# Kernel optimization log

Hardware: AMD Instinct MI355X
Metric: run time of the kernel (lower is better)

## Reference

```python
import jax, jax.numpy as jnp
import numpy as np

C, W, H = 256, 64, 192
RECORD_LEN = np.array([5, 3, 4, 2, 5, 3, 4, 2], dtype=np.int64)  # sums to 28


def setup_inputs() -> dict:
    key = jax.random.key(0)
    total = int(RECORD_LEN.sum())
    x = jax.random.normal(key, (total, C, W, H), dtype=jnp.float32)
    record_len = jnp.asarray(RECORD_LEN)
    return {"x": x, "record_len": record_len}


def _group_attention(xx):
    # xx: [L, C, W, H] -> per-pixel self-attention over the L agents, d_model = C
    L = xx.shape[0]
    q = xx.reshape(L, C, W * H).transpose(2, 0, 1)          # [N=W*H, L, C]
    score = jnp.einsum('nlc,nmc->nlm', q, q) / jnp.sqrt(jnp.float32(C))
    attn = jax.nn.softmax(score, axis=-1)                    # [N, L, L]
    # original keeps only ego agent (row 0) of the context
    ctx0 = jnp.einsum('nm,nmc->nc', attn[:, 0, :], q)        # [N, C]
    out = ctx0.T.reshape(1, C, W, H)
    attn_maps = attn.transpose(1, 2, 0).reshape(L, L, W, H)
    return out, attn_maps


def reference(x, record_len):
    rl = np.asarray(record_len)  # static ragged lengths
    offsets = np.concatenate([[0], np.cumsum(rl)])
    outs = []
    attn_last = None
    for i in range(len(rl)):  # small fixed number of ragged groups
        xx = x[int(offsets[i]):int(offsets[i + 1])]
        out_i, attn_last = _group_attention(xx)
        outs.append(out_i)
    # matches torch: returns fused ego features per scene + attn of LAST group
    return jnp.concatenate(outs, axis=0), attn_last
```

## Files before the change

kernel.cpp:

```cpp
#include <hip/hip_runtime.h>
#include <hip/hip_bf16.h>
#include <math.h>

#define C_DIM 256
#define W_DIM 64
#define H_DIM 192
#define WH (W_DIM * H_DIM)
#define NGROUPS 8
#define BLOCKS_PER_GROUP (WH / 256)

template <int L, bool WRITE_ATTN>
__device__ __forceinline__ void att_group_body(
    const float* __restrict__ xg,
    float* __restrict__ out,
    float* __restrict__ attn_out,
    int n)
{
    constexpr int NTRI = L * (L + 1) / 2;
    float s[NTRI];
#pragma unroll
    for (int i = 0; i < NTRI; ++i) s[i] = 0.0f;

#pragma unroll 4
    for (int c = 0; c < C_DIM; ++c) {
        float v[L];
#pragma unroll
        for (int l = 0; l < L; ++l)
            v[l] = xg[(l * C_DIM + c) * WH + n];
        int idx = 0;
#pragma unroll
        for (int l = 0; l < L; ++l)
#pragma unroll
            for (int m = l; m < L; ++m)
                s[idx++] += v[l] * v[m];
    }

    const float scale = 0.0625f;

    float p0[L];
    float mx = -INFINITY;
#pragma unroll
    for (int m = 0; m < L; ++m) {
        p0[m] = s[m] * scale;
        mx = fmaxf(mx, p0[m]);
    }
    float sum = 0.0f;
#pragma unroll
    for (int m = 0; m < L; ++m) {
        p0[m] = __expf(p0[m] - mx);
        sum += p0[m];
    }
    const float inv = 1.0f / sum;
#pragma unroll
    for (int m = 0; m < L; ++m) p0[m] *= inv;

    if constexpr (WRITE_ATTN) {
        float g[L][L];
        int idx = 0;
#pragma unroll
        for (int l = 0; l < L; ++l)
#pragma unroll
            for (int m = l; m < L; ++m) {
                const float v = s[idx++] * scale;
                g[l][m] = v;
                g[m][l] = v;
            }
#pragma unroll
        for (int l = 0; l < L; ++l) {
            float mx2 = -INFINITY;
#pragma unroll
            for (int m = 0; m < L; ++m) mx2 = fmaxf(mx2, g[l][m]);
            float e[L];
            float sm = 0.0f;
#pragma unroll
            for (int m = 0; m < L; ++m) {
                e[m] = __expf(g[l][m] - mx2);
                sm += e[m];
            }
            const float iv = 1.0f / sm;
#pragma unroll
            for (int m = 0; m < L; ++m)
                attn_out[(l * L + m) * WH + n] = e[m] * iv;
        }
    }

#pragma unroll 4
    for (int c = 0; c < C_DIM; ++c) {
        float acc = 0.0f;
#pragma unroll
        for (int m = 0; m < L; ++m)
            acc += p0[m] * xg[(m * C_DIM + c) * WH + n];
        out[c * WH + n] = acc;
    }
}

__global__ __launch_bounds__(256) void att_fused_kernel(
    const float* __restrict__ x,
    float* __restrict__ out0,
    float* __restrict__ attn)
{
    const int b = blockIdx.x;
    const int g = b / BLOCKS_PER_GROUP;
    const int bn = b - g * BLOCKS_PER_GROUP;
    const int n = bn * 256 + threadIdx.x;

    const int offs[NGROUPS] = {0, 5, 8, 12, 14, 19, 22, 26};
    const int lens[NGROUPS] = {5, 3, 4, 2, 5, 3, 4, 2};

    const float* xg = x + (size_t)offs[g] * C_DIM * WH;
    float* og = out0 + (size_t)g * C_DIM * WH;

    switch (lens[g]) {
        case 5: att_group_body<5, false>(xg, og, nullptr, n); break;
        case 4: att_group_body<4, false>(xg, og, nullptr, n); break;
        case 3: att_group_body<3, false>(xg, og, nullptr, n); break;
        case 2:
            if (g == NGROUPS - 1)
                att_group_body<2, true>(xg, og, attn, n);
            else
                att_group_body<2, false>(xg, og, nullptr, n);
            break;
    }
}

extern "C" void kernel_launch(void* const* d_in, const int* in_sizes, int n_in,
                              void* d_out, int out_size, void* d_ws, size_t ws_size,
                              hipStream_t stream) {
    const float* x = (const float*)d_in[0];
    float* out0 = (float*)d_out;
    float* attn = out0 + (size_t)NGROUPS * C_DIM * WH;

    const dim3 grid(NGROUPS * BLOCKS_PER_GROUP);
    const dim3 block(256);
    att_fused_kernel<<<grid, block, 0, stream>>>(x, out0, attn);
}
```

Before: 564.9 us.

## Rewrite as persistent cooperative kernel splitting channels across blocks with flag sync

```diff
diff --git a/kernel.cpp b/kernel.cpp
--- a/kernel.cpp
+++ b/kernel.cpp
@@ -1,125 +1,296 @@
 #include <hip/hip_runtime.h>
-#include <hip/hip_bf16.h>
 #include <math.h>
 
 #define C_DIM 256
-#define W_DIM 64
-#define H_DIM 192
-#define WH (W_DIM * H_DIM)
+#define WH 12288
+#define WH4 3072
 #define NGROUPS 8
-#define BLOCKS_PER_GROUP (WH / 256)
-
-template <int L, bool WRITE_ATTN>
-__device__ __forceinline__ void att_group_body(
-    const float* __restrict__ xg,
-    float* __restrict__ out,
-    float* __restrict__ attn_out,
-    int n)
+#define STEPS 12
+#define NBLOCKS 256
+#define SLOT_V4 160
+#define SCALE 0.0625f
+
+typedef float v4 __attribute__((ext_vector_type(4)));
+
+__device__ __forceinline__ v4 v4max(v4 a, v4 b) {
+    v4 r; r[0]=fmaxf(a[0],b[0]); r[1]=fmaxf(a[1],b[1]);
+    r[2]=fmaxf(a[2],b[2]); r[3]=fmaxf(a[3],b[3]); return r;
+}
+__device__ __forceinline__ v4 v4exp(v4 a) {
+    v4 r; r[0]=__expf(a[0]); r[1]=__expf(a[1]);
+    r[2]=__expf(a[2]); r[3]=__expf(a[3]); return r;
+}
+
+__device__ __forceinline__ void load_slab(
+    v4 (&sl)[5][2], const v4* __restrict__ x4, int item, int cl, int nsub)
 {
-    constexpr int NTRI = L * (L + 1) / 2;
-    float s[NTRI];
-#pragma unroll
-    for (int i = 0; i < NTRI; ++i) s[i] = 0.0f;
-
-#pragma unroll 4
-    for (int c = 0; c < C_DIM; ++c) {
-        float v[L];
-#pragma unroll
-        for (int l = 0; l < L; ++l)
-            v[l] = xg[(l * C_DIM + c) * WH + n];
-        int idx = 0;
-#pragma unroll
-        for (int l = 0; l < L; ++l)
-#pragma unroll
-            for (int m = l; m < L; ++m)
-                s[idx++] += v[l] * v[m];
-    }
-
-    const float scale = 0.0625f;
-
-    float p0[L];
-    float mx = -INFINITY;
-#pragma unroll
-    for (int m = 0; m < L; ++m) {
-        p0[m] = s[m] * scale;
-        mx = fmaxf(mx, p0[m]);
-    }
-    float sum = 0.0f;
-#pragma unroll
-    for (int m = 0; m < L; ++m) {
-        p0[m] = __expf(p0[m] - mx);
-        sum += p0[m];
-    }
-    const float inv = 1.0f / sum;
-#pragma unroll
-    for (int m = 0; m < L; ++m) p0[m] *= inv;
-
-    if constexpr (WRITE_ATTN) {
-        float g[L][L];
-        int idx = 0;
-#pragma unroll
-        for (int l = 0; l < L; ++l)
-#pragma unroll
-            for (int m = l; m < L; ++m) {
-                const float v = s[idx++] * scale;
-                g[l][m] = v;
-                g[m][l] = v;
-            }
-#pragma unroll
-        for (int l = 0; l < L; ++l) {
-            float mx2 = -INFINITY;
-#pragma unroll
-            for (int m = 0; m < L; ++m) mx2 = fmaxf(mx2, g[l][m]);
-            float e[L];
-            float sm = 0.0f;
-#pragma unroll
-            for (int m = 0; m < L; ++m) {
-                e[m] = __expf(g[l][m] - mx2);
-                sm += e[m];
-            }
-            const float iv = 1.0f / sm;
+    const int offs_[8] = {0, 5, 8, 12, 14, 19, 22, 26};
+    const int lens_[8] = {5, 3, 4, 2, 5, 3, 4, 2};
+    const int g = item / 384;
+    const int r = item - g * 384;
+    const int bn = r >> 2;
+    const int chunk = r & 3;
+    const int L = lens_[g];
+    const size_t base = ((size_t)offs_[g] * C_DIM + chunk * 64 + cl) * WH4
+                        + bn * 32 + nsub;
+#pragma unroll
+    for (int l = 0; l < 5; ++l) {
+        if (l < L) {
+#pragma unroll
+            for (int j = 0; j < 2; ++j)
+                sl[l][j] = __builtin_nontemporal_load(
+                    &x4[base + (size_t)l * C_DIM * WH4 + 16 * j]);
+        }
+    }
+}
+
+template <int L, bool ATTN>
+__device__ __forceinline__ void step(
+    v4 (&slab)[5][2], v4 (&slabN)[5][2],
+    const v4* __restrict__ x4, v4* __restrict__ out4, v4* __restrict__ attn4,
+    int* __restrict__ flags, v4* __restrict__ slots,
+    v4* __restrict__ stg, v4* __restrict__ fin,
+    const int s, const int b, const bool pf,
+    const int wave, const int lane, const int cl, const int nsub)
+{
+    constexpr int NACC = ATTN ? 3 : L;
+    const int item = s * NBLOCKS + b;
+    const int g = item / 384;
+    const int r = item - g * 384;
+    const int bn = r >> 2;
+    const int chunk = r & 3;
+    const int n4 = bn * 32 + nsub;
+
+    v4 acc[NACC][2];
+#pragma unroll
+    for (int j = 0; j < 2; ++j) {
+        if constexpr (ATTN) {
+            acc[0][j] = slab[0][j] * slab[0][j];
+            acc[1][j] = slab[0][j] * slab[1][j];
+            acc[2][j] = slab[1][j] * slab[1][j];
+        } else {
 #pragma unroll
             for (int m = 0; m < L; ++m)
-                attn_out[(l * L + m) * WH + n] = e[m] * iv;
-        }
-    }
-
-#pragma unroll 4
-    for (int c = 0; c < C_DIM; ++c) {
-        float acc = 0.0f;
-#pragma unroll
-        for (int m = 0; m < L; ++m)
-            acc += p0[m] * xg[(m * C_DIM + c) * WH + n];
-        out[c * WH + n] = acc;
-    }
-}
-
-__global__ __launch_bounds__(256) void att_fused_kernel(
+                acc[m][j] = slab[0][j] * slab[m][j];
+        }
+    }
+
+#pragma unroll
+    for (int i = 0; i < NACC; ++i)
+#pragma unroll
+        for (int j = 0; j < 2; ++j) {
+            v4 t;
+#pragma unroll
+            for (int q = 0; q < 4; ++q) t[q] = __shfl_xor(acc[i][j][q], 16);
+            acc[i][j] += t;
+#pragma unroll
+            for (int q = 0; q < 4; ++q) t[q] = __shfl_xor(acc[i][j][q], 32);
+            acc[i][j] += t;
+        }
+
+    if (lane < 16) {
+#pragma unroll
+        for (int i = 0; i < NACC; ++i)
+#pragma unroll
+            for (int j = 0; j < 2; ++j)
+                stg[((wave * 5 + i) * 2 + j) * 16 + lane] = acc[i][j];
+    }
+
+    if (pf) load_slab(slabN, x4, item + NBLOCKS, cl, nsub);
+
+    __syncthreads();
+
+    if (wave == 0) {
+        const int part = lane >> 4;
+        const int t = lane & 15;
+        v4 blk[NACC][2];
+#pragma unroll
+        for (int i = 0; i < NACC; ++i)
+#pragma unroll
+            for (int j = 0; j < 2; ++j) {
+                v4 a = stg[(((part * 4 + 0) * 5 + i) * 2 + j) * 16 + t];
+#pragma unroll
+                for (int w = 1; w < 4; ++w)
+                    a += stg[(((part * 4 + w) * 5 + i) * 2 + j) * 16 + t];
+                blk[i][j] = a;
+            }
+#pragma unroll
+        for (int i = 0; i < NACC; ++i)
+#pragma unroll
+            for (int j = 0; j < 2; ++j) {
+                v4 tv;
+#pragma unroll
+                for (int q = 0; q < 4; ++q) tv[q] = __shfl_xor(blk[i][j][q], 16);
+                blk[i][j] += tv;
+#pragma unroll
+                for (int q = 0; q < 4; ++q) tv[q] = __shfl_xor(blk[i][j][q], 32);
+                blk[i][j] += tv;
+            }
+        v4* slot = slots + (size_t)item * SLOT_V4;
+        if (lane < 16) {
+#pragma unroll
+            for (int i = 0; i < NACC; ++i)
+#pragma unroll
+                for (int j = 0; j < 2; ++j)
+                    slot[(i * 2 + j) * 16 + lane] = blk[i][j];
+        }
+        int* fb = flags + s * NBLOCKS + (b & ~3);
+        if (lane == 0) {
+            __hip_atomic_store(fb + chunk, 1, __ATOMIC_RELEASE,
+                               __HIP_MEMORY_SCOPE_AGENT);
+            int it = 0;
+            for (;;) {
+                int ok = 1;
+#pragma unroll
+                for (int k = 0; k < 4; ++k)
+                    ok &= (__hip_atomic_load(fb + k, __ATOMIC_ACQUIRE,
+                                             __HIP_MEMORY_SCOPE_AGENT) == 1);
+                if (ok || ++it > (1 << 24)) break;
+                __builtin_amdgcn_s_sleep(2);
+            }
+        }
+        const v4* qb = slots + (size_t)(s * NBLOCKS + (b & ~3)) * SLOT_V4;
+        v4 fs[NACC][2];
+#pragma unroll
+        for (int i = 0; i < NACC; ++i)
+#pragma unroll
+            for (int j = 0; j < 2; ++j)
+                fs[i][j] = qb[(size_t)part * SLOT_V4 + (i * 2 + j) * 16 + t];
+#pragma unroll
+        for (int i = 0; i < NACC; ++i)
+#pragma unroll
+            for (int j = 0; j < 2; ++j) {
+                v4 tv;
+#pragma unroll
+                for (int q = 0; q < 4; ++q) tv[q] = __shfl_xor(fs[i][j][q], 16);
+                fs[i][j] += tv;
+#pragma unroll
+                for (int q = 0; q < 4; ++q) tv[q] = __shfl_xor(fs[i][j][q], 32);
+                fs[i][j] += tv;
+            }
+        if (lane < 16) {
+#pragma unroll
+            for (int i = 0; i < NACC; ++i)
+#pragma unroll
+                for (int j = 0; j < 2; ++j)
+                    fin[(i * 2 + j) * 16 + lane] = fs[i][j];
+        }
+    }
+    __syncthreads();
+
+    v4 sf[NACC][2];
+#pragma unroll
+    for (int i = 0; i < NACC; ++i)
+#pragma unroll
+        for (int j = 0; j < 2; ++j)
+            sf[i][j] = fin[(i * 2 + j) * 16 + nsub];
+
+    v4 p[L][2];
+    v4 mx[2] = {(v4)(-INFINITY), (v4)(-INFINITY)};
+#pragma unroll
+    for (int m = 0; m < L; ++m)
+#pragma unroll
+        for (int j = 0; j < 2; ++j) {
+            p[m][j] = sf[m][j] * SCALE;
+            mx[j] = v4max(mx[j], p[m][j]);
+        }
+    v4 sum[2] = {(v4)0.0f, (v4)0.0f};
+#pragma unroll
+    for (int m = 0; m < L; ++m)
+#pragma unroll
+        for (int j = 0; j < 2; ++j) {
+            p[m][j] = v4exp(p[m][j] - mx[j]);
+            sum[j] += p[m][j];
+        }
+    v4 inv[2];
+#pragma unroll
+    for (int j = 0; j < 2; ++j)
+#pragma unroll
+        for (int q = 0; q < 4; ++q) inv[j][q] = 1.0f / sum[j][q];
+
+    const size_t orow = (size_t)(g * C_DIM + chunk * 64 + cl) * WH4 + n4;
+#pragma unroll
+    for (int j = 0; j < 2; ++j) {
+        v4 o = (v4)0.0f;
+#pragma unroll
+        for (int m = 0; m < L; ++m) o += (p[m][j] * inv[j]) * slab[m][j];
+        __builtin_nontemporal_store(o, &out4[orow + 16 * j]);
+    }
+
+    if constexpr (ATTN) {
+        if (chunk == 0 && cl < 2) {
+            const int rr = cl;
+#pragma unroll
+            for (int j = 0; j < 2; ++j) {
+                v4 a0 = (rr == 0 ? sf[0][j] : sf[1][j]) * SCALE;
+                v4 a1 = (rr == 0 ? sf[1][j] : sf[2][j]) * SCALE;
+                v4 mm = v4max(a0, a1);
+                v4 e0 = v4exp(a0 - mm), e1 = v4exp(a1 - mm);
+                v4 iv;
+#pragma unroll
+                for (int q = 0; q < 4; ++q) iv[q] = 1.0f / (e0[q] + e1[q]);
+                __builtin_nontemporal_store(
+                    e0 * iv, &attn4[(size_t)(rr * 2 + 0) * WH4 + n4 + 16 * j]);
+                __builtin_nontemporal_store(
+                    e1 * iv, &attn4[(size_t)(rr * 2 + 1) * WH4 + n4 + 16 * j]);
+            }
+        }
+    }
+
+    if (pf) {
+#pragma unroll
+        for (int l = 0; l < 5; ++l)
+#pragma unroll
+            for (int j = 0; j < 2; ++j)
+                slab[l][j] = slabN[l][j];
+    }
+}
+
+__global__ __launch_bounds__(1024, 4) void att_coop_kernel(
     const float* __restrict__ x,
     float* __restrict__ out0,
-    float* __restrict__ attn)
+    float* __restrict__ attnp,
+    int* __restrict__ ws)
 {
+    __shared__ v4 stg[16 * 5 * 2 * 16];
+    __shared__ v4 fin[5 * 2 * 16];
+
     const int b = blockIdx.x;
-    const int g = b / BLOCKS_PER_GROUP;
-    const int bn = b - g * BLOCKS_PER_GROUP;
-    const int n = bn * 256 + threadIdx.x;
-
-    const int offs[NGROUPS] = {0, 5, 8, 12, 14, 19, 22, 26};
-    const int lens[NGROUPS] = {5, 3, 4, 2, 5, 3, 4, 2};
-
-    const float* xg = x + (size_t)offs[g] * C_DIM * WH;
-    float* og = out0 + (size_t)g * C_DIM * WH;
-
-    switch (lens[g]) {
-        case 5: att_group_body<5, false>(xg, og, nullptr, n); break;
-        case 4: att_group_body<4, false>(xg, og, nullptr, n); break;
-        case 3: att_group_body<3, false>(xg, og, nullptr, n); break;
-        case 2:
+    const int tid = threadIdx.x;
+    const int wave = tid >> 6;
+    const int lane = tid & 63;
+    const int cl = wave * 4 + (lane >> 4);
+    const int nsub = lane & 15;
+
+    const v4* x4 = reinterpret_cast<const v4*>(x);
+    v4* out4 = reinterpret_cast<v4*>(out0);
+    v4* attn4 = reinterpret_cast<v4*>(attnp);
+    int* flags = ws;
+    v4* slots = reinterpret_cast<v4*>((char*)ws + 16384);
+
+    v4 slab[5][2], slabN[5][2];
+    load_slab(slab, x4, b, cl, nsub);
+
+    const int lens_[8] = {5, 3, 4, 2, 5, 3, 4, 2};
+    for (int s = 0; s < STEPS; ++s) {
+        const int item = s * NBLOCKS + b;
+        const int g = item / 384;
+        const bool pf = (s + 1 < STEPS);
+        switch (lens_[g]) {
+        case 5: step<5, false>(slab, slabN, x4, out4, attn4, flags, slots,
+                               stg, fin, s, b, pf, wave, lane, cl, nsub); break;
+        case 4: step<4, false>(slab, slabN, x4, out4, attn4, flags, slots,
+                               stg, fin, s, b, pf, wave, lane, cl, nsub); break;
+        case 3: step<3, false>(slab, slabN, x4, out4, attn4, flags, slots,
+                               stg, fin, s, b, pf, wave, lane, cl, nsub); break;
+        default:
             if (g == NGROUPS - 1)
-                att_group_body<2, true>(xg, og, attn, n);
+                step<2, true>(slab, slabN, x4, out4, attn4, flags, slots,
+                              stg, fin, s, b, pf, wave, lane, cl, nsub);
             else
-                att_group_body<2, false>(xg, og, nullptr, n);
-            break;
+                step<2, false>(slab, slabN, x4, out4, attn4, flags, slots,
+                               stg, fin, s, b, pf, wave, lane, cl, nsub);
+        }
     }
 }
 
@@ -129,8 +300,8 @@
     const float* x = (const float*)d_in[0];
     float* out0 = (float*)d_out;
     float* attn = out0 + (size_t)NGROUPS * C_DIM * WH;
-
-    const dim3 grid(NGROUPS * BLOCKS_PER_GROUP);
-    const dim3 block(256);
-    att_fused_kernel<<<grid, block, 0, stream>>>(x, out0, attn);
-}
+    int* ws = (int*)d_ws;
+
+    hipMemsetAsync(ws, 0, 16384, stream);
+    att_coop_kernel<<<dim3(NBLOCKS), dim3(1024), 0, stream>>>(x, out0, attn, ws);
+}
```

Result: slower. 1.030 ms (+82.4%).
